# Performance work log

Hardware: AMD Instinct MI355X
Metric: run time of the kernel (lower is better)

The kernel has to match this reference:

```python
import jax, jax.numpy as jnp
import numpy as np

N_NODES = 100000
N_EDGES = 3200000
IN_SIZE = 128
HID = 128
OUT = 64
HEADS = (4, 1)
NEG_SLOPE = 0.2  # DGL GATConv default leaky_relu slope


def setup_inputs() -> dict:
    key = jax.random.key(0)
    ks = jax.random.split(key, 10)
    x = jax.random.normal(ks[0], (N_NODES, IN_SIZE), dtype=jnp.float32)
    src = jax.random.randint(ks[1], (N_EDGES,), 0, N_NODES, dtype=jnp.int64)
    dst = jax.random.randint(ks[2], (N_EDGES,), 0, N_NODES, dtype=jnp.int64)
    s1 = 1.0 / np.sqrt(IN_SIZE)
    s2 = 1.0 / np.sqrt(HID * HEADS[0])
    W1 = jax.random.normal(ks[3], (IN_SIZE, HEADS[0] * HID), dtype=jnp.float32) * s1
    al1 = jax.random.normal(ks[4], (HEADS[0], HID), dtype=jnp.float32) * 0.1
    ar1 = jax.random.normal(ks[5], (HEADS[0], HID), dtype=jnp.float32) * 0.1
    W2 = jax.random.normal(ks[6], (HEADS[0] * HID, HEADS[1] * OUT), dtype=jnp.float32) * s2
    al2 = jax.random.normal(ks[7], (HEADS[1], OUT), dtype=jnp.float32) * 0.1
    ar2 = jax.random.normal(ks[8], (HEADS[1], OUT), dtype=jnp.float32) * 0.1
    return {"x": x, "W1": W1, "al1": al1, "ar1": ar1, "W2": W2,
            "al2": al2, "ar2": ar2, "src": src, "dst": dst}


def gat_conv(h, W, al, ar, src, dst, n_heads, d_out):
    # h: (N, F_in); W: (F_in, n_heads*d_out); al/ar: (n_heads, d_out)
    n = h.shape[0]
    feat = (h @ W).reshape(n, n_heads, d_out)          # (N, H, D)
    el = jnp.sum(feat * al, axis=-1)                    # (N, H) source score
    er = jnp.sum(feat * ar, axis=-1)                    # (N, H) dest score
    e = jax.nn.leaky_relu(el[src] + er[dst], NEG_SLOPE)  # (E, H)
    # edge softmax over incoming edges of each destination node
    m = jax.ops.segment_max(e, dst, num_segments=n)     # (N, H)
    m = jnp.where(jnp.isfinite(m), m, 0.0)              # nodes with no in-edges
    ex = jnp.exp(e - m[dst])                            # (E, H)
    s = jax.ops.segment_sum(ex, dst, num_segments=n)    # (N, H)
    alpha = ex / s[dst]                                 # (E, H); s[dst]>0 always
    msg = alpha[:, :, None] * feat[src]                 # (E, H, D)
    out = jax.ops.segment_sum(msg, dst, num_segments=n)  # (N, H, D)
    return out


def reference(x, W1, al1, ar1, W2, al2, ar2, src, dst):
    n = x.shape[0]
    h = gat_conv(x, W1, al1, ar1, src, dst, HEADS[0], HID)   # (N, H1, HID)
    h = jax.nn.elu(h).reshape(n, HEADS[0] * HID)             # flatten(1)
    h = gat_conv(h, W2, al2, ar2, src, dst, HEADS[1], OUT)   # (N, H2, OUT)
    h = h.reshape(n * HEADS[1], OUT)                          # view(N*H2, OUT)
    return h
```

## Files before the change

### kernel.cpp

```cpp
#include <hip/hip_runtime.h>
#include <math.h>

#define N_NODES 100000
#define N_EDGES 3200000
#define NEG 0.2f
#define NPB 128
#define NB  782
#define CAP 4608
#define LOG2E 1.442695041f

typedef __attribute__((ext_vector_type(8))) short short8;
typedef __attribute__((ext_vector_type(4))) float f32x4;
typedef __attribute__((ext_vector_type(2))) float f32x2;

__device__ __forceinline__ float bflo(unsigned int u){
  union { unsigned int i; float f; } v; v.i = u << 16; return v.f;
}
__device__ __forceinline__ float bfhi(unsigned int u){
  union { unsigned int i; float f; } v; v.i = u & 0xffff0000u; return v.f;
}
__device__ __forceinline__ unsigned short f2bf(float f){
  union { float f; unsigned int i; } v; v.f = f;
  unsigned int r = v.i + 0x7fffu + ((v.i >> 16) & 1u);
  return (unsigned short)(r >> 16);
}
__device__ __forceinline__ unsigned int packbf(float lo, float hi){
  return (unsigned int)f2bf(lo) | ((unsigned int)f2bf(hi) << 16);
}
__device__ __forceinline__ void pk_fma(f32x2 &acc, f32x2 a, f32x2 w){
  asm("v_pk_fma_f32 %0, %1, %2, %0" : "+v"(acc) : "v"(a), "v"(w));
}
__device__ __forceinline__ float wexp(float t){
  return __builtin_amdgcn_exp2f(fmaxf(t, NEG * t));
}
__device__ __forceinline__ f32x4 wexp4(f32x4 t){
  f32x4 r; r[0]=wexp(t[0]); r[1]=wexp(t[1]); r[2]=wexp(t[2]); r[3]=wexp(t[3]);
  return r;
}
__device__ __forceinline__ void fma_x8(f32x2 (*acc)[4], uint4 q, f32x4 w){
  f32x2 p0,p1,p2,p3;
  p0[0]=bflo(q.x); p0[1]=bfhi(q.x);
  p1[0]=bflo(q.y); p1[1]=bfhi(q.y);
  p2[0]=bflo(q.z); p2[1]=bfhi(q.z);
  p3[0]=bflo(q.w); p3[1]=bfhi(q.w);
  #pragma unroll
  for (int h=0;h<4;++h){
    f32x2 W; W[0]=w[h]; W[1]=w[h];
    pk_fma(acc[h][0], p0, W);
    pk_fma(acc[h][1], p1, W);
    pk_fma(acc[h][2], p2, W);
    pk_fma(acc[h][3], p3, W);
  }
}

__global__ void k_prep(const float* __restrict__ W1, const float* __restrict__ W2,
                       const float* __restrict__ al1, const float* __restrict__ ar1,
                       unsigned short* __restrict__ W1t, unsigned short* __restrict__ W2t,
                       int* __restrict__ bcur, float* __restrict__ val,
                       float* __restrict__ var){
  int i = blockIdx.x*256 + threadIdx.x;
  if (i < 65536){ int n = i >> 7, k = i & 127; W1t[i] = f2bf(W1[k*512 + n]); }
  else if (i < 98304){ int j = i - 65536; int n = j >> 9, k = j & 511; W2t[j] = f2bf(W2[k*64 + n]); }
  else if (i < 98304 + NB){ int b = i - 98304; bcur[b*16] = b*CAP; }
  else if (i >= 99328 && i < 99840){
    int j = i - 99328; int k = j >> 2, h = j & 3;
    float s = 0.f;
    for (int d=0; d<128; ++d) s += W1[k*512 + h*128 + d] * al1[h*128 + d];
    val[j] = s;
  } else if (i >= 99840 && i < 100352){
    int j = i - 99840; int k = j >> 2, h = j & 3;
    float s = 0.f;
    for (int d=0; d<128; ++d) s += W1[k*512 + h*128 + d] * ar1[h*128 + d];
    var[j] = s;
  }
}

__global__ __launch_bounds__(256) void k_xcvt(const float* __restrict__ x,
    const float* __restrict__ val, const float* __restrict__ var,
    unsigned short* __restrict__ xb, float* __restrict__ el, float* __restrict__ er){
  int wave = threadIdx.x >> 6, lane = threadIdx.x & 63;
  int q = lane >> 4, ql = lane & 15;
  int n = (blockIdx.x*4 + wave)*4 + q;
  f32x4 valr[8], varr[8];
  #pragma unroll
  for (int j=0;j<8;++j){
    valr[j] = *(const f32x4*)(val + (ql*8+j)*4);
    varr[j] = *(const f32x4*)(var + (ql*8+j)*4);
  }
  const float* xp = x + (size_t)n*128 + ql*8;
  float4 xa = *(const float4*)xp;
  float4 xc = *(const float4*)(xp + 4);
  uint4 o; o.x = packbf(xa.x,xa.y); o.y = packbf(xa.z,xa.w);
  o.z = packbf(xc.x,xc.y); o.w = packbf(xc.z,xc.w);
  *(uint4*)(xb + (size_t)n*128 + ql*8) = o;
  float xs[8] = {xa.x,xa.y,xa.z,xa.w,xc.x,xc.y,xc.z,xc.w};
  f32x4 e4; e4[0]=0.f; e4[1]=0.f; e4[2]=0.f; e4[3]=0.f;
  f32x4 r4 = e4;
  #pragma unroll
  for (int j=0;j<8;++j){
    e4 += valr[j] * xs[j];
    r4 += varr[j] * xs[j];
  }
  #pragma unroll
  for (int m=1;m<16;m<<=1){
    #pragma unroll
    for (int c=0;c<4;++c){
      e4[c] += __shfl_xor(e4[c], m);
      r4[c] += __shfl_xor(r4[c], m);
    }
  }
  if (ql == 0){
    f32x4 es = e4 * LOG2E, rs = r4 * LOG2E;
    *(f32x4*)(el + n*4) = es;
    *(f32x4*)(er + n*4) = rs;
  }
}

__global__ void k_bucket(const int* __restrict__ src, const int* __restrict__ dst,
                         int* __restrict__ bcur, int* __restrict__ staged){
  int e = blockIdx.x*blockDim.x + threadIdx.x;
  if (e < N_EDGES){
    int d = dst[e];
    int b = d >> 7;
    int pos = atomicAdd(&bcur[b*16], 1);
    staged[pos] = (src[e] << 7) | (d & (NPB-1));
  }
}
__global__ __launch_bounds__(1024) void k_bscan(const int* __restrict__ bcur,
    int* __restrict__ bbase){
  __shared__ int lds[1024];
  int t = threadIdx.x;
  int v = (t < NB) ? (bcur[t*16] - t*CAP) : 0;
  lds[t] = v; __syncthreads();
  for (int off=1; off<1024; off<<=1){
    int u = (t>=off)? lds[t-off] : 0;
    __syncthreads();
    lds[t] += u;
    __syncthreads();
  }
  if (t < NB) bbase[t] = lds[t] - v;
  if (t == 0) bbase[NB] = N_EDGES;
}
__global__ __launch_bounds__(256) void k_binsort(const int* __restrict__ staged,
    const int* __restrict__ bcur, const int* __restrict__ bbase,
    int* __restrict__ csr_src, int* __restrict__ indptr){
  __shared__ int hist[NPB];
  __shared__ int scan[NPB];
  __shared__ int lcur[NPB];
  const int b = blockIdx.x, t = threadIdx.x;
  const int st0 = b*CAP;
  const int cnt = bcur[b*16] - st0;
  const int obase = bbase[b];
  if (t < NPB) hist[t] = 0;
  __syncthreads();
  for (int i = t; i < cnt; i += 256)
    atomicAdd(&hist[staged[st0 + i] & (NPB-1)], 1);
  __syncthreads();
  int v = (t < NPB) ? hist[t] : 0;
  if (t < NPB) scan[t] = v;
  __syncthreads();
  for (int off=1; off<NPB; off<<=1){
    int u = (t < NPB && t >= off) ? scan[t-off] : 0;
    __syncthreads();
    if (t < NPB) scan[t] += u;
    __syncthreads();
  }
  const int node0 = b * NPB;
  if (t < NPB){
    int ex = obase + scan[t] - v;
    lcur[t] = ex;
    if (node0 + t < N_NODES) indptr[node0 + t] = ex;
  }
  if (b == NB-1 && t == 0) indptr[N_NODES] = N_EDGES;
  __syncthreads();
  for (int i = t; i < cnt; i += 256){
    int pv = staged[st0 + i];
    int pos = atomicAdd(&lcur[pv & (NPB-1)], 1);
    csr_src[pos] = pv >> 7;
  }
}

__global__ __launch_bounds__(256) void k_agg1(const unsigned short* __restrict__ xb,
    const float* __restrict__ el, const float* __restrict__ er,
    const int* __restrict__ indptr, const int* __restrict__ csr_src,
    unsigned short* __restrict__ sagg, float* __restrict__ ssumA){
  int wave = threadIdx.x >> 6, lane = threadIdx.x & 63;
  int n = blockIdx.x*4 + wave;
  if (n >= N_NODES) return;
  int p0 = indptr[n], p1 = indptr[n+1];
  const int q = lane >> 4, ql = lane & 15;
  f32x4 er4 = *(const f32x4*)(er + n*4);
  f32x4 ss; ss[0]=0.f; ss[1]=0.f; ss[2]=0.f; ss[3]=0.f;
  f32x2 acc[4][4];
  #pragma unroll
  for (int h=0;h<4;++h)
    #pragma unroll
    for (int j=0;j<4;++j){ acc[h][j][0]=0.f; acc[h][j][1]=0.f; }
  int e = p0;
  for (; e + 15 < p1; e += 16){
    int s0 = csr_src[e + 0  + q];
    int s1 = csr_src[e + 4  + q];
    int s2 = csr_src[e + 8  + q];
    int s3 = csr_src[e + 12 + q];
    uint4 q0 = *(const uint4*)(xb + (size_t)s0*128 + ql*8);
    uint4 q1 = *(const uint4*)(xb + (size_t)s1*128 + ql*8);
    uint4 q2 = *(const uint4*)(xb + (size_t)s2*128 + ql*8);
    uint4 q3 = *(const uint4*)(xb + (size_t)s3*128 + ql*8);
    f32x4 e0 = *(const f32x4*)(el + s0*4);
    f32x4 e1 = *(const f32x4*)(el + s1*4);
    f32x4 e2 = *(const f32x4*)(el + s2*4);
    f32x4 e3 = *(const f32x4*)(el + s3*4);
    f32x4 w0 = wexp4(e0 + er4);
    f32x4 w1 = wexp4(e1 + er4);
    f32x4 w2 = wexp4(e2 + er4);
    f32x4 w3 = wexp4(e3 + er4);
    ss += (w0 + w1) + (w2 + w3);
    fma_x8(acc, q0, w0);
    fma_x8(acc, q1, w1);
    fma_x8(acc, q2, w2);
    fma_x8(acc, q3, w3);
  }
  for (; e < p1; e += 4){
    int idx = e + q;
    bool ok = idx < p1;
    int s = csr_src[ok ? idx : e];
    uint4 qq = *(const uint4*)(xb + (size_t)s*128 + ql*8);
    f32x4 ee = *(const f32x4*)(el + s*4);
    f32x4 w = wexp4(ee + er4);
    if (!ok){ w[0]=0.f; w[1]=0.f; w[2]=0.f; w[3]=0.f; }
    ss += w;
    fma_x8(acc, qq, w);
  }
  #pragma unroll
  for (int m=16;m<64;m<<=1){
    #pragma unroll
    for (int c=0;c<4;++c) ss[c] += __shfl_xor(ss[c], m);
    #pragma unroll
    for (int h=0;h<4;++h)
      #pragma unroll
      for (int j=0;j<4;++j){
        acc[h][j][0] += __shfl_xor(acc[h][j][0], m);
        acc[h][j][1] += __shfl_xor(acc[h][j][1], m);
      }
  }
  if (q == 0){
    unsigned short* op = sagg + (size_t)n*512 + ql*8;
    #pragma unroll
    for (int h=0;h<4;++h){
      uint4 o;
      o.x = packbf(acc[h][0][0], acc[h][0][1]);
      o.y = packbf(acc[h][1][0], acc[h][1][1]);
      o.z = packbf(acc[h][2][0], acc[h][2][1]);
      o.w = packbf(acc[h][3][0], acc[h][3][1]);
      *(uint4*)(op + h*128) = o;
    }
    if (ql == 0) *(f32x4*)(ssumA + n*4) = ss;
  }
}

__global__ __launch_bounds__(256) void k_mmpost(unsigned short* __restrict__ sagg,
    const unsigned short* __restrict__ Bt, const float* __restrict__ ssumA, int M){
  __shared__ unsigned short sm[18432];
  unsigned short* As = sm;
  unsigned short* Bs = sm + 9216;
  const int t = threadIdx.x;
  const int w = t >> 6, l = t & 63;
  const int quad = l >> 4, l16 = l & 15;
  const int m0 = blockIdx.x * 128;
  const int h = blockIdx.y;
  const int moff = (w & 1) * 64, noff = (w >> 1) * 64;
  f32x4 acc[4][4];
  #pragma unroll
  for (int i=0;i<4;++i)
    #pragma unroll
    for (int j=0;j<4;++j){ acc[i][j][0]=0.f; acc[i][j][1]=0.f; acc[i][j][2]=0.f; acc[i][j][3]=0.f; }
  for (int kb = 0; kb < 2; ++kb){
    const int K0 = kb * 64;
    #pragma unroll
    for (int i=0;i<4;++i){
      int idx = t + i*256;
      int row = idx >> 3, c8 = (idx & 7) * 8;
      uint4 v; v.x=0u; v.y=0u; v.z=0u; v.w=0u;
      if (m0 + row < M)
        v = *(const uint4*)(sagg + (size_t)(m0+row)*512 + h*128 + K0 + c8);
      *(uint4*)(As + row*72 + c8) = v;
    }
    #pragma unroll
    for (int i=0;i<4;++i){
      int idx = t + i*256;
      int row = idx >> 3, c8 = (idx & 7) * 8;
      *(uint4*)(Bs + row*72 + c8) =
        *(const uint4*)(Bt + (size_t)(h*128 + row)*128 + K0 + c8);
    }
    __syncthreads();
    #pragma unroll
    for (int ks = 0; ks < 2; ++ks){
      short8 af[4], bfr[4];
      #pragma unroll
      for (int mi=0; mi<4; ++mi)
        af[mi] = *(const short8*)(As + (moff + mi*16 + l16)*72 + ks*32 + quad*8);
      #pragma unroll
      for (int ni=0; ni<4; ++ni)
        bfr[ni] = *(const short8*)(Bs + (noff + ni*16 + l16)*72 + ks*32 + quad*8);
      #pragma unroll
      for (int mi=0; mi<4; ++mi)
        #pragma unroll
        for (int ni=0; ni<4; ++ni)
          acc[mi][ni] = __builtin_amdgcn_mfma_f32_16x16x32_bf16(af[mi], bfr[ni], acc[mi][ni], 0,0,0);
    }
    __syncthreads();
  }
  float invr[4][4];
  #pragma unroll
  for (int mi=0; mi<4; ++mi)
    #pragma unroll
    for (int r=0;r<4;++r){
      int gr = m0 + moff + mi*16 + quad*4 + r;
      float s = (gr < M) ? ssumA[gr*4 + h] : 0.f;
      invr[mi][r] = s > 0.f ? 1.f/s : 0.f;
    }
  unsigned short* Cs = sm;
  #pragma unroll
  for (int mi=0; mi<4; ++mi)
    #pragma unroll
    for (int ni=0; ni<4; ++ni){
      int col = noff + ni*16 + l16;
      int rb  = moff + mi*16 + quad*4;
      #pragma unroll
      for (int r=0;r<4;++r){
        float v = acc[mi][ni][r] * invr[mi][r];
        v = v > 0.f ? v : __expf(v) - 1.f;
        Cs[(rb+r)*136 + col] = f2bf(v);
      }
    }
  __syncthreads();
  #pragma unroll
  for (int i=0;i<8;++i){
    int e = t + i*256;
    int row = e >> 4, c8 = (e & 15) * 8;
    if (m0 + row < M)
      *(uint4*)(sagg + (size_t)(m0+row)*512 + h*128 + c8) =
        *(const uint4*)(Cs + row*136 + c8);
  }
}

__global__ __launch_bounds__(256) void k_mm2(const unsigned short* __restrict__ A,
    const unsigned short* __restrict__ Bt,
    unsigned short* __restrict__ C, int M,
    const float* __restrict__ al, const float* __restrict__ ar,
    float* __restrict__ el, float* __restrict__ er){
  __shared__ unsigned short sm[13824];
  unsigned short* As = sm;
  unsigned short* Bs = sm + 9216;
  const int t = threadIdx.x;
  const int w = t >> 6, l = t & 63;
  const int quad = l >> 4, l16 = l & 15;
  const int m0 = blockIdx.x * 128;
  const int moff = w * 32;
  f32x4 acc[2][4];
  #pragma unroll
  for (int i=0;i<2;++i)
    #pragma unroll
    for (int j=0;j<4;++j){ acc[i][j][0]=0.f; acc[i][j][1]=0.f; acc[i][j][2]=0.f; acc[i][j][3]=0.f; }
  for (int kb = 0; kb < 8; ++kb){
    const int K0 = kb * 64;
    #pragma unroll
    for (int i=0;i<4;++i){
      int idx = t + i*256;
      int row = idx >> 3, c8 = (idx & 7) * 8;
      uint4 v; v.x=0u; v.y=0u; v.z=0u; v.w=0u;
      if (m0 + row < M) v = *(const uint4*)(A + (size_t)(m0+row)*512 + K0 + c8);
      *(uint4*)(As + row*72 + c8) = v;
    }
    #pragma unroll
    for (int i=0;i<2;++i){
      int idx = t + i*256;
      int row = idx >> 3, c8 = (idx & 7) * 8;
      *(uint4*)(Bs + row*72 + c8) = *(const uint4*)(Bt + (size_t)row*512 + K0 + c8);
    }
    __syncthreads();
    #pragma unroll
    for (int ks = 0; ks < 2; ++ks){
      short8 af[2], bfr[4];
      #pragma unroll
      for (int mi=0; mi<2; ++mi)
        af[mi] = *(const short8*)(As + (moff + mi*16 + l16)*72 + ks*32 + quad*8);
      #pragma unroll
      for (int ni=0; ni<4; ++ni)
        bfr[ni] = *(const short8*)(Bs + (ni*16 + l16)*72 + ks*32 + quad*8);
      #pragma unroll
      for (int mi=0; mi<2; ++mi)
        #pragma unroll
        for (int ni=0; ni<4; ++ni)
          acc[mi][ni] = __builtin_amdgcn_mfma_f32_16x16x32_bf16(af[mi], bfr[ni], acc[mi][ni], 0,0,0);
    }
    __syncthreads();
  }
  unsigned short* Cs = sm;
  #pragma unroll
  for (int mi=0; mi<2; ++mi)
    #pragma unroll
    for (int ni=0; ni<4; ++ni){
      int col = ni*16 + l16;
      int rb  = moff + mi*16 + quad*4;
      #pragma unroll
      for (int r=0;r<4;++r) Cs[(rb+r)*72 + col] = f2bf(acc[mi][ni][r]);
    }
  __syncthreads();
  #pragma unroll
  for (int i=0;i<4;++i){
    int e = t + i*256;
    int row = e >> 3, c8 = (e & 7) * 8;
    if (m0 + row < M)
      *(uint4*)(C + (size_t)(m0+row)*64 + c8) = *(const uint4*)(Cs + row*72 + c8);
  }
  {
    int row = t >> 1, half = t & 1;
    const float* alp = al + half*32;
    const float* arp = ar + half*32;
    const unsigned short* cp = Cs + row*72 + half*32;
    float se = 0.f, sr = 0.f;
    #pragma unroll
    for (int i=0;i<4;++i){
      uint4 q = *(const uint4*)(cp + i*8);
      float4 a0 = *(const float4*)(alp + i*8), a1 = *(const float4*)(alp + i*8 + 4);
      float4 r0 = *(const float4*)(arp + i*8), r1 = *(const float4*)(arp + i*8 + 4);
      se += bflo(q.x)*a0.x + bfhi(q.x)*a0.y + bflo(q.y)*a0.z + bfhi(q.y)*a0.w
          + bflo(q.z)*a1.x + bfhi(q.z)*a1.y + bflo(q.w)*a1.z + bfhi(q.w)*a1.w;
      sr += bflo(q.x)*r0.x + bfhi(q.x)*r0.y + bflo(q.y)*r0.z + bfhi(q.y)*r0.w
          + bflo(q.z)*r1.x + bfhi(q.z)*r1.y + bflo(q.w)*r1.z + bfhi(q.w)*r1.w;
    }
    se += __shfl_xor(se, 1); sr += __shfl_xor(sr, 1);
    if (half == 0 && m0 + row < M){
      el[m0+row] = se * LOG2E;
      er[m0+row] = sr * LOG2E;
    }
  }
}

__global__ __launch_bounds__(256) void k_agg2(const unsigned short* __restrict__ feat,
    const float* __restrict__ el, const float* __restrict__ er,
    const int* __restrict__ indptr, const int* __restrict__ csr_src,
    float* __restrict__ out){
  int wave = threadIdx.x >> 6, lane = threadIdx.x & 63;
  int n = blockIdx.x*4 + wave;
  if (n >= N_NODES) return;
  int p0 = indptr[n], p1 = indptr[n+1];
  float ern = er[n];
  int g = lane >> 3, ql = lane & 7;
  float s = 0.f;
  f32x2 acc[4];
  #pragma unroll
  for (int i=0;i<4;++i){ acc[i][0]=0.f; acc[i][1]=0.f; }
  int e = p0 + g;
  for (; e + 8 < p1; e += 16){
    int sa = csr_src[e], sb = csr_src[e+8];
    uint4 va = *(const uint4*)(feat + (size_t)sa*64 + ql*8);
    uint4 vb = *(const uint4*)(feat + (size_t)sb*64 + ql*8);
    float wa = wexp(el[sa] + ern);
    float wb = wexp(el[sb] + ern);
    s += wa + wb;
    f32x2 Wa; Wa[0]=wa; Wa[1]=wa;
    f32x2 Wb; Wb[0]=wb; Wb[1]=wb;
    f32x2 a;
    a[0]=bflo(va.x); a[1]=bfhi(va.x); pk_fma(acc[0], a, Wa);
    a[0]=bflo(va.y); a[1]=bfhi(va.y); pk_fma(acc[1], a, Wa);
    a[0]=bflo(va.z); a[1]=bfhi(va.z); pk_fma(acc[2], a, Wa);
    a[0]=bflo(va.w); a[1]=bfhi(va.w); pk_fma(acc[3], a, Wa);
    a[0]=bflo(vb.x); a[1]=bfhi(vb.x); pk_fma(acc[0], a, Wb);
    a[0]=bflo(vb.y); a[1]=bfhi(vb.y); pk_fma(acc[1], a, Wb);
    a[0]=bflo(vb.z); a[1]=bfhi(vb.z); pk_fma(acc[2], a, Wb);
    a[0]=bflo(vb.w); a[1]=bfhi(vb.w); pk_fma(acc[3], a, Wb);
  }
  for (; e < p1; e += 8){
    int si = csr_src[e];
    float w = wexp(el[si] + ern);
    uint4 v = *(const uint4*)(feat + (size_t)si*64 + ql*8);
    s += w;
    f32x2 W; W[0]=w; W[1]=w;
    f32x2 a;
    a[0]=bflo(v.x); a[1]=bfhi(v.x); pk_fma(acc[0], a, W);
    a[0]=bflo(v.y); a[1]=bfhi(v.y); pk_fma(acc[1], a, W);
    a[0]=bflo(v.z); a[1]=bfhi(v.z); pk_fma(acc[2], a, W);
    a[0]=bflo(v.w); a[1]=bfhi(v.w); pk_fma(acc[3], a, W);
  }
  #pragma unroll
  for (int m=8;m<64;m<<=1){
    s += __shfl_xor(s,m);
    #pragma unroll
    for (int i=0;i<4;++i){
      acc[i][0] += __shfl_xor(acc[i][0],m);
      acc[i][1] += __shfl_xor(acc[i][1],m);
    }
  }
  float inv = s > 0.f ? 1.f/s : 0.f;
  if (g == 0){
    float* op = out + (size_t)n*64 + ql*8;
    *(float4*)op     = make_float4(acc[0][0]*inv, acc[0][1]*inv, acc[1][0]*inv, acc[1][1]*inv);
    *(float4*)(op+4) = make_float4(acc[2][0]*inv, acc[2][1]*inv, acc[3][0]*inv, acc[3][1]*inv);
  }
}

extern "C" void kernel_launch(void* const* d_in, const int* in_sizes, int n_in,
                              void* d_out, int out_size, void* d_ws, size_t ws_size,
                              hipStream_t stream){
  const float* x   = (const float*)d_in[0];
  const float* W1  = (const float*)d_in[1];
  const float* al1 = (const float*)d_in[2];
  const float* ar1 = (const float*)d_in[3];
  const float* W2  = (const float*)d_in[4];
  const float* al2 = (const float*)d_in[5];
  const float* ar2 = (const float*)d_in[6];
  const int* src   = (const int*)d_in[7];
  const int* dst   = (const int*)d_in[8];
  float* out = (float*)d_out;

  char* ws = (char*)d_ws;
  size_t off = 0;
  auto alloc = [&](size_t bytes)->char*{
    char* p = ws + off; off += (bytes + 255) & ~(size_t)255; return p;
  };
  unsigned short* xbuf = (unsigned short*)alloc((size_t)N_NODES*128*2);
  unsigned short* sagg = (unsigned short*)alloc((size_t)N_NODES*512*2);
  float* ssumA = (float*)alloc((size_t)N_NODES*4*4);
  unsigned short* W1t = (unsigned short*)alloc(512*128*2);
  unsigned short* W2t = (unsigned short*)alloc(64*512*2);
  float* val  = (float*)alloc(512*4);
  float* var  = (float*)alloc(512*4);
  float* el1 = (float*)alloc((size_t)N_NODES*4*4);
  float* er1 = (float*)alloc((size_t)N_NODES*4*4);
  float* el2 = el1;
  float* er2 = er1;
  int* bcur    = (int*)alloc((size_t)NB*16*4);
  int* bbase   = (int*)alloc((size_t)(NB+1)*4);
  int* indptr  = (int*)alloc((size_t)(N_NODES+1)*4);
  int* staged  = (int*)alloc((size_t)NB*CAP*4);
  int* csr_src = (int*)alloc((size_t)N_EDGES*4);
  unsigned short* feat2b = (unsigned short*)staged;

  dim3 b256(256);
  k_prep<<<dim3(392), b256, 0, stream>>>(W1, W2, al1, ar1, W1t, W2t, bcur, val, var);
  k_xcvt<<<dim3(6250), b256, 0, stream>>>(x, val, var, xbuf, el1, er1);
  k_bucket<<<dim3((N_EDGES+255)/256), b256, 0, stream>>>(src, dst, bcur, staged);
  k_bscan<<<dim3(1), dim3(1024), 0, stream>>>(bcur, bbase);
  k_binsort<<<dim3(NB), b256, 0, stream>>>(staged, bcur, bbase, csr_src, indptr);
  k_agg1<<<dim3(25000), b256, 0, stream>>>(xbuf, el1, er1, indptr, csr_src, sagg, ssumA);
  k_mmpost<<<dim3(782, 4), b256, 0, stream>>>(sagg, W1t, ssumA, N_NODES);
  k_mm2<<<dim3(782), b256, 0, stream>>>(sagg, W2t, feat2b, N_NODES, al2, ar2, el2, er2);
  k_agg2<<<dim3(25000), b256, 0, stream>>>(feat2b, el2, er2, indptr, csr_src, out);
}
```

Before: 680.8 us.

## Fold bucket scan into binsort, use 32-bit address math, unroll agg2 deeper

Removes the single-block k_bscan launch: each binsort block now sums the preceding bucket counts itself through a shared-memory reduction, saving a launch and a serialized kernel at the cost of redundant reads of bcur. The gather kernels compute addresses with unsigned 32-bit shifts on byte pointers instead of size_t multiplies, which should cut 64-bit address instructions. k_agg2 unrolls its edge loop from 2 to 4 gathers per lane to keep more loads in flight, using more registers.

Measured after the change: 687.6 us. No clear change (+1.0%).

```diff
diff --git a/kernel.cpp b/kernel.cpp
--- a/kernel.cpp
+++ b/kernel.cpp
@@ -126,33 +126,26 @@
     staged[pos] = (src[e] << 7) | (d & (NPB-1));
   }
 }
-__global__ __launch_bounds__(1024) void k_bscan(const int* __restrict__ bcur,
-    int* __restrict__ bbase){
-  __shared__ int lds[1024];
-  int t = threadIdx.x;
-  int v = (t < NB) ? (bcur[t*16] - t*CAP) : 0;
-  lds[t] = v; __syncthreads();
-  for (int off=1; off<1024; off<<=1){
-    int u = (t>=off)? lds[t-off] : 0;
-    __syncthreads();
-    lds[t] += u;
-    __syncthreads();
-  }
-  if (t < NB) bbase[t] = lds[t] - v;
-  if (t == 0) bbase[NB] = N_EDGES;
-}
 __global__ __launch_bounds__(256) void k_binsort(const int* __restrict__ staged,
-    const int* __restrict__ bcur, const int* __restrict__ bbase,
-    int* __restrict__ csr_src, int* __restrict__ indptr){
+    const int* __restrict__ bcur, int* __restrict__ csr_src,
+    int* __restrict__ indptr){
   __shared__ int hist[NPB];
   __shared__ int scan[NPB];
   __shared__ int lcur[NPB];
+  __shared__ int red[256];
   const int b = blockIdx.x, t = threadIdx.x;
   const int st0 = b*CAP;
   const int cnt = bcur[b*16] - st0;
-  const int obase = bbase[b];
+  int part = 0;
+  for (int i = t; i < b; i += 256) part += bcur[i*16] - i*CAP;
+  red[t] = part;
   if (t < NPB) hist[t] = 0;
   __syncthreads();
+  for (int off = 128; off > 0; off >>= 1){
+    if (t < off) red[t] += red[t + off];
+    __syncthreads();
+  }
+  const int obase = red[0];
   for (int i = t; i < cnt; i += 256)
     atomicAdd(&hist[staged[st0 + i] & (NPB-1)], 1);
   __syncthreads();
@@ -189,6 +182,9 @@
   if (n >= N_NODES) return;
   int p0 = indptr[n], p1 = indptr[n+1];
   const int q = lane >> 4, ql = lane & 15;
+  const unsigned d0 = ql * 16u;
+  const char* xbb = (const char*)xb;
+  const char* elb = (const char*)el;
   f32x4 er4 = *(const f32x4*)(er + n*4);
   f32x4 ss; ss[0]=0.f; ss[1]=0.f; ss[2]=0.f; ss[3]=0.f;
   f32x2 acc[4][4];
@@ -198,18 +194,18 @@
     for (int j=0;j<4;++j){ acc[h][j][0]=0.f; acc[h][j][1]=0.f; }
   int e = p0;
   for (; e + 15 < p1; e += 16){
-    int s0 = csr_src[e + 0  + q];
-    int s1 = csr_src[e + 4  + q];
-    int s2 = csr_src[e + 8  + q];
-    int s3 = csr_src[e + 12 + q];
-    uint4 q0 = *(const uint4*)(xb + (size_t)s0*128 + ql*8);
-    uint4 q1 = *(const uint4*)(xb + (size_t)s1*128 + ql*8);
-    uint4 q2 = *(const uint4*)(xb + (size_t)s2*128 + ql*8);
-    uint4 q3 = *(const uint4*)(xb + (size_t)s3*128 + ql*8);
-    f32x4 e0 = *(const f32x4*)(el + s0*4);
-    f32x4 e1 = *(const f32x4*)(el + s1*4);
-    f32x4 e2 = *(const f32x4*)(el + s2*4);
-    f32x4 e3 = *(const f32x4*)(el + s3*4);
+    unsigned s0 = (unsigned)csr_src[e + 0  + q];
+    unsigned s1 = (unsigned)csr_src[e + 4  + q];
+    unsigned s2 = (unsigned)csr_src[e + 8  + q];
+    unsigned s3 = (unsigned)csr_src[e + 12 + q];
+    uint4 q0 = *(const uint4*)(xbb + (s0 << 8) + d0);
+    uint4 q1 = *(const uint4*)(xbb + (s1 << 8) + d0);
+    uint4 q2 = *(const uint4*)(xbb + (s2 << 8) + d0);
+    uint4 q3 = *(const uint4*)(xbb + (s3 << 8) + d0);
+    f32x4 e0 = *(const f32x4*)(elb + (s0 << 4));
+    f32x4 e1 = *(const f32x4*)(elb + (s1 << 4));
+    f32x4 e2 = *(const f32x4*)(elb + (s2 << 4));
+    f32x4 e3 = *(const f32x4*)(elb + (s3 << 4));
     f32x4 w0 = wexp4(e0 + er4);
     f32x4 w1 = wexp4(e1 + er4);
     f32x4 w2 = wexp4(e2 + er4);
@@ -223,9 +219,9 @@
   for (; e < p1; e += 4){
     int idx = e + q;
     bool ok = idx < p1;
-    int s = csr_src[ok ? idx : e];
-    uint4 qq = *(const uint4*)(xb + (size_t)s*128 + ql*8);
-    f32x4 ee = *(const f32x4*)(el + s*4);
+    unsigned s = (unsigned)csr_src[ok ? idx : e];
+    uint4 qq = *(const uint4*)(xbb + (s << 8) + d0);
+    f32x4 ee = *(const f32x4*)(elb + (s << 4));
     f32x4 w = wexp4(ee + er4);
     if (!ok){ w[0]=0.f; w[1]=0.f; w[2]=0.f; w[3]=0.f; }
     ss += w;
@@ -448,37 +444,56 @@
   int p0 = indptr[n], p1 = indptr[n+1];
   float ern = er[n];
   int g = lane >> 3, ql = lane & 7;
+  const unsigned d0 = ql * 16u;
+  const char* fb  = (const char*)feat;
+  const char* elb = (const char*)el;
   float s = 0.f;
   f32x2 acc[4];
   #pragma unroll
   for (int i=0;i<4;++i){ acc[i][0]=0.f; acc[i][1]=0.f; }
   int e = p0 + g;
-  for (; e + 8 < p1; e += 16){
-    int sa = csr_src[e], sb = csr_src[e+8];
-    uint4 va = *(const uint4*)(feat + (size_t)sa*64 + ql*8);
-    uint4 vb = *(const uint4*)(feat + (size_t)sb*64 + ql*8);
-    float wa = wexp(el[sa] + ern);
-    float wb = wexp(el[sb] + ern);
-    s += wa + wb;
-    f32x2 Wa; Wa[0]=wa; Wa[1]=wa;
-    f32x2 Wb; Wb[0]=wb; Wb[1]=wb;
-    f32x2 a;
-    a[0]=bflo(va.x); a[1]=bfhi(va.x); pk_fma(acc[0], a, Wa);
-    a[0]=bflo(va.y); a[1]=bfhi(va.y); pk_fma(acc[1], a, Wa);
-    a[0]=bflo(va.z); a[1]=bfhi(va.z); pk_fma(acc[2], a, Wa);
-    a[0]=bflo(va.w); a[1]=bfhi(va.w); pk_fma(acc[3], a, Wa);
-    a[0]=bflo(vb.x); a[1]=bfhi(vb.x); pk_fma(acc[0], a, Wb);
-    a[0]=bflo(vb.y); a[1]=bfhi(vb.y); pk_fma(acc[1], a, Wb);
-    a[0]=bflo(vb.z); a[1]=bfhi(vb.z); pk_fma(acc[2], a, Wb);
-    a[0]=bflo(vb.w); a[1]=bfhi(vb.w); pk_fma(acc[3], a, Wb);
+  for (; e + 24 < p1; e += 32){
+    unsigned sa = (unsigned)csr_src[e];
+    unsigned sb = (unsigned)csr_src[e+8];
+    unsigned sc = (unsigned)csr_src[e+16];
+    unsigned sd = (unsigned)csr_src[e+24];
+    uint4 va = *(const uint4*)(fb + (sa << 7) + d0);
+    uint4 vb = *(const uint4*)(fb + (sb << 7) + d0);
+    uint4 vc = *(const uint4*)(fb + (sc << 7) + d0);
+    uint4 vd = *(const uint4*)(fb + (sd << 7) + d0);
+    float wa = wexp(*(const float*)(elb + (sa << 2)) + ern);
+    float wb = wexp(*(const float*)(elb + (sb << 2)) + ern);
+    float wc = wexp(*(const float*)(elb + (sc << 2)) + ern);
+    float wd = wexp(*(const float*)(elb + (sd << 2)) + ern);
+    s += (wa + wb) + (wc + wd);
+    f32x2 W, a;
+    W[0]=wa; W[1]=wa;
+    a[0]=bflo(va.x); a[1]=bfhi(va.x); pk_fma(acc[0], a, W);
+    a[0]=bflo(va.y); a[1]=bfhi(va.y); pk_fma(acc[1], a, W);
+    a[0]=bflo(va.z); a[1]=bfhi(va.z); pk_fma(acc[2], a, W);
+    a[0]=bflo(va.w); a[1]=bfhi(va.w); pk_fma(acc[3], a, W);
+    W[0]=wb; W[1]=wb;
+    a[0]=bflo(vb.x); a[1]=bfhi(vb.x); pk_fma(acc[0], a, W);
+    a[0]=bflo(vb.y); a[1]=bfhi(vb.y); pk_fma(acc[1], a, W);
+    a[0]=bflo(vb.z); a[1]=bfhi(vb.z); pk_fma(acc[2], a, W);
+    a[0]=bflo(vb.w); a[1]=bfhi(vb.w); pk_fma(acc[3], a, W);
+    W[0]=wc; W[1]=wc;
+    a[0]=bflo(vc.x); a[1]=bfhi(vc.x); pk_fma(acc[0], a, W);
+    a[0]=bflo(vc.y); a[1]=bfhi(vc.y); pk_fma(acc[1], a, W);
+    a[0]=bflo(vc.z); a[1]=bfhi(vc.z); pk_fma(acc[2], a, W);
+    a[0]=bflo(vc.w); a[1]=bfhi(vc.w); pk_fma(acc[3], a, W);
+    W[0]=wd; W[1]=wd;
+    a[0]=bflo(vd.x); a[1]=bfhi(vd.x); pk_fma(acc[0], a, W);
+    a[0]=bflo(vd.y); a[1]=bfhi(vd.y); pk_fma(acc[1], a, W);
+    a[0]=bflo(vd.z); a[1]=bfhi(vd.z); pk_fma(acc[2], a, W);
+    a[0]=bflo(vd.w); a[1]=bfhi(vd.w); pk_fma(acc[3], a, W);
   }
   for (; e < p1; e += 8){
-    int si = csr_src[e];
-    float w = wexp(el[si] + ern);
-    uint4 v = *(const uint4*)(feat + (size_t)si*64 + ql*8);
+    unsigned si = (unsigned)csr_src[e];
+    float w = wexp(*(const float*)(elb + (si << 2)) + ern);
+    uint4 v = *(const uint4*)(fb + (si << 7) + d0);
     s += w;
-    f32x2 W; W[0]=w; W[1]=w;
-    f32x2 a;
+    f32x2 W, a; W[0]=w; W[1]=w;
     a[0]=bflo(v.x); a[1]=bfhi(v.x); pk_fma(acc[0], a, W);
     a[0]=bflo(v.y); a[1]=bfhi(v.y); pk_fma(acc[1], a, W);
     a[0]=bflo(v.z); a[1]=bfhi(v.z); pk_fma(acc[2], a, W);
@@ -532,7 +547,6 @@
   float* el2 = el1;
   float* er2 = er1;
   int* bcur    = (int*)alloc((size_t)NB*16*4);
-  int* bbase   = (int*)alloc((size_t)(NB+1)*4);
   int* indptr  = (int*)alloc((size_t)(N_NODES+1)*4);
   int* staged  = (int*)alloc((size_t)NB*CAP*4);
   int* csr_src = (int*)alloc((size_t)N_EDGES*4);
@@ -542,8 +556,7 @@
   k_prep<<<dim3(392), b256, 0, stream>>>(W1, W2, al1, ar1, W1t, W2t, bcur, val, var);
   k_xcvt<<<dim3(6250), b256, 0, stream>>>(x, val, var, xbuf, el1, er1);
   k_bucket<<<dim3((N_EDGES+255)/256), b256, 0, stream>>>(src, dst, bcur, staged);
-  k_bscan<<<dim3(1), dim3(1024), 0, stream>>>(bcur, bbase);
-  k_binsort<<<dim3(NB), b256, 0, stream>>>(staged, bcur, bbase, csr_src, indptr);
+  k_binsort<<<dim3(NB), b256, 0, stream>>>(staged, bcur, csr_src, indptr);
   k_agg1<<<dim3(25000), b256, 0, stream>>>(xbuf, el1, er1, indptr, csr_src, sagg, ssumA);
   k_mmpost<<<dim3(782, 4), b256, 0, stream>>>(sagg, W1t, ssumA, N_NODES);
   k_mm2<<<dim3(782), b256, 0, stream>>>(sagg, W2t, feat2b, N_NODES, al2, ar2, el2, er2);
```
